# Kernel optimization log

Measured on AMD Instinct MI355X. Metric: run time of the kernel, lower is better.

The kernel has to match this reference:

```python
import jax, jax.numpy as jnp
import numpy as np

B, S, D_MODEL, N_HEADS, D_K, D_V = 32, 512, 256, 16, 16, 16


def setup_inputs() -> dict:
    key = jax.random.key(0)
    ks = jax.random.split(key, 9)
    def xavier(k, fan_in, fan_out):
        lim = np.sqrt(6.0 / (fan_in + fan_out)).astype(np.float32)
        return jax.random.uniform(k, (fan_out, fan_in), jnp.float32, -lim, lim)
    return {
        "Q": jax.random.normal(ks[0], (B, S, D_MODEL), jnp.float32),
        "K": jax.random.normal(ks[1], (B, S, D_MODEL), jnp.float32),
        "V": jax.random.normal(ks[2], (B, S, D_MODEL), jnp.float32),
        "mask": jnp.ones((B, S), jnp.float32),
        "W_Q": xavier(ks[3], D_MODEL, N_HEADS * D_K),
        "b_Q": jnp.zeros((N_HEADS * D_K,), jnp.float32),
        "W_K": xavier(ks[4], D_MODEL, N_HEADS * D_K),
        "b_K": jnp.zeros((N_HEADS * D_K,), jnp.float32),
        "W_V": xavier(ks[5], D_MODEL, N_HEADS * D_V),
        "b_V": jnp.zeros((N_HEADS * D_V,), jnp.float32),
    }


def reference(Q, K, V, mask, W_Q, b_Q, W_K, b_K, W_V, b_V):
    # Projections: torch Linear stores weight as (out, in) -> x @ W.T + b
    def proj(x, W, b, d):
        y = jnp.einsum('bsd,ed->bse', x, W) + b  # [B,S,H*d]
        return y.reshape(B, S, N_HEADS, d).transpose(0, 2, 1, 3)  # [B,H,S,d]
    q = proj(Q, W_Q, b_Q, D_K)
    k = proj(K, W_K, b_K, D_K)
    v = proj(V, W_V, b_V, D_V)
    # Unstabilized exp-score attention with multiplicative mask
    scores = jnp.exp(jnp.einsum('bhqd,bhkd->bhqk', q, k) / np.sqrt(D_K).astype(np.float32))
    scores = scores * mask[:, None, None, :]  # mask over key axis
    attn = scores / (jnp.sum(scores, axis=-1, keepdims=True) + 1e-8)
    ctx = jnp.einsum('bhqk,bhkd->bhqd', attn, v)  # [B,H,S,D_V]
    return ctx.transpose(0, 2, 1, 3).reshape(B, S, N_HEADS * D_V)
```

## Files before the change

kernel.cpp:

```cpp
#include <hip/hip_runtime.h>
#include <hip/hip_bf16.h>


#define PROJ_ELEMS (32 * 16 * 512 * 16)
#define LOG2E 1.44269504088896f

typedef _Float16 f16x4 __attribute__((ext_vector_type(4)));
typedef float    f32x4 __attribute__((ext_vector_type(4)));

static __device__ __forceinline__ f16x4 cvt4(float4 v) {
    f16x4 r;
    r[0] = (_Float16)v.x; r[1] = (_Float16)v.y;
    r[2] = (_Float16)v.z; r[3] = (_Float16)v.w;
    return r;
}

__global__ __launch_bounds__(256, 3) void proj_mfma(
    const float* __restrict__ Qx, const float* __restrict__ Kx, const float* __restrict__ Vx,
    const float* __restrict__ WQ, const float* __restrict__ bQ,
    const float* __restrict__ WK, const float* __restrict__ bK,
    const float* __restrict__ WV, const float* __restrict__ bV,
    _Float16* __restrict__ qh, _Float16* __restrict__ kh, _Float16* __restrict__ vth)
{
    const int proj = blockIdx.z;
    const float* __restrict__ X  = (proj == 0) ? Qx : (proj == 1) ? Kx : Vx;
    const float* __restrict__ W  = (proj == 0) ? WQ : (proj == 1) ? WK : WV;
    const float* __restrict__ bb = (proj == 0) ? bQ : (proj == 1) ? bK : bV;

    const int row0 = blockIdx.x * 64;
    const int t = threadIdx.x;
    const int w = t >> 6, l = t & 63;
    const int lm16 = l & 15, lg = l >> 4;

    __shared__ _Float16 xs[64][72];
    __shared__ _Float16 wsh[256][72];
    __shared__ float bl[256];

    bl[t] = bb[t];

    f32x4 acc[4][4];
#pragma unroll
    for (int mi = 0; mi < 4; mi++)
#pragma unroll
        for (int ni = 0; ni < 4; ni++) acc[mi][ni] = (f32x4){0.f, 0.f, 0.f, 0.f};

    for (int k0 = 0; k0 < 256; k0 += 64) {
        __syncthreads();
#pragma unroll
        for (int i = 0; i < 4; i++) {
            int f4 = t + i * 256;
            int r = f4 >> 4, kq = f4 & 15;
            float4 xv = *(const float4*)&X[(size_t)(row0 + r) * 256 + k0 + kq * 4];
            *(f16x4*)&xs[r][kq * 4] = cvt4(xv);
        }
#pragma unroll
        for (int i = 0; i < 16; i++) {
            int f4 = t + i * 256;
            int r = f4 >> 4, kq = f4 & 15;
            float4 wv = *(const float4*)&W[(size_t)r * 256 + k0 + kq * 4];
            *(f16x4*)&wsh[r][kq * 4] = cvt4(wv);
        }
        __syncthreads();

#pragma unroll
        for (int kq = 0; kq < 4; kq++) {
            f16x4 xf[4], wf[4];
#pragma unroll
            for (int mi = 0; mi < 4; mi++)
                xf[mi] = *(const f16x4*)&xs[mi * 16 + lm16][kq * 16 + lg * 4];
#pragma unroll
            for (int ni = 0; ni < 4; ni++)
                wf[ni] = *(const f16x4*)&wsh[w * 64 + ni * 16 + lm16][kq * 16 + lg * 4];

            if (proj < 2) {
#pragma unroll
                for (int mi = 0; mi < 4; mi++)
#pragma unroll
                    for (int ni = 0; ni < 4; ni++)
                        acc[mi][ni] = __builtin_amdgcn_mfma_f32_16x16x16f16(
                            wf[ni], xf[mi], acc[mi][ni], 0, 0, 0);
            } else {
#pragma unroll
                for (int mi = 0; mi < 4; mi++)
#pragma unroll
                    for (int ni = 0; ni < 4; ni++)
                        acc[mi][ni] = __builtin_amdgcn_mfma_f32_16x16x16f16(
                            xf[mi], wf[ni], acc[mi][ni], 0, 0, 0);
            }
        }
    }

    const int bq = row0 >> 9;
    const int sbase = row0 & 511;

    if (proj < 2) {
        const float scl = (proj == 0) ? 0.25f * LOG2E : 1.0f;
        _Float16* __restrict__ outp = (proj == 0) ? qh : kh;
#pragma unroll
        for (int mi = 0; mi < 4; mi++) {
            const int s = sbase + mi * 16 + lm16;
#pragma unroll
            for (int ni = 0; ni < 4; ni++) {
                const int col0 = w * 64 + ni * 16 + lg * 4;
                const int h = col0 >> 4, d0 = col0 & 15;
                _Float16 tmp[4];
#pragma unroll
                for (int r = 0; r < 4; r++)
                    tmp[r] = (_Float16)((acc[mi][ni][r] + bl[col0 + r]) * scl);
                *(f16x4*)&outp[(((size_t)bq * 16 + h) * 512 + s) * 16 + d0] =
                    *(const f16x4*)tmp;
            }
        }
    } else {
#pragma unroll
        for (int mi = 0; mi < 4; mi++) {
            const int s0 = sbase + mi * 16 + lg * 4;
#pragma unroll
            for (int ni = 0; ni < 4; ni++) {
                const int col = w * 64 + ni * 16 + lm16;
                const int h = col >> 4, d = col & 15;
                const float bc = bl[col];
                _Float16 tmp[4];
#pragma unroll
                for (int r = 0; r < 4; r++)
                    tmp[r] = (_Float16)(acc[mi][ni][r] + bc);
                *(f16x4*)&vth[(((size_t)bq * 16 + h) * 16 + d) * 512 + s0] =
                    *(const f16x4*)tmp;
            }
        }
    }
}

__global__ __launch_bounds__(256, 4) void attn_mfma(
    const _Float16* __restrict__ qh, const _Float16* __restrict__ kh,
    const _Float16* __restrict__ vth, const float* __restrict__ mask,
    float* __restrict__ out)
{
    const int blk  = blockIdx.x;
    const int bh   = blk >> 1;
    const int half = blk & 1;
    const int b = bh >> 4, h = bh & 15;

    __shared__ _Float16 ks[512 * 16];
    __shared__ _Float16 vt[16 * 528];
    __shared__ float    lm[512];
    __shared__ float    sums[256];

    const int t = threadIdx.x;
    const int w = t >> 6, l = t & 63;
    const int lm16 = l & 15, lg = l >> 4;

    {
        const float4* src = (const float4*)(kh + (size_t)bh * 8192);
        float4* dst = (float4*)ks;
#pragma unroll
        for (int i = 0; i < 4; i++) dst[t + i * 256] = src[t + i * 256];
    }
    {
        const _Float16* src = vth + (size_t)bh * 8192;
#pragma unroll
        for (int i = 0; i < 4; i++) {
            int f = t + i * 256;
            int d = f >> 6, c = f & 63;
            *(float4*)&vt[d * 528 + c * 8] = *(const float4*)&src[d * 512 + c * 8];
        }
    }
    {
#pragma unroll
        for (int i = 0; i < 2; i++) {
            int j = t + i * 256;
            lm[j] = __builtin_amdgcn_logf(mask[b * 512 + j]);
        }
    }

    f16x4 qf[4];
    {
        const _Float16* qb = qh + (size_t)bh * 8192;
#pragma unroll
        for (int mt = 0; mt < 4; mt++) {
            int m = half * 256 + w * 64 + mt * 16 + lm16;
            qf[mt] = *(const f16x4*)&qb[m * 16 + lg * 4];
        }
    }

    f32x4 acc[4];
    float rs[4];
#pragma unroll
    for (int mt = 0; mt < 4; mt++) {
        acc[mt] = (f32x4){0.f, 0.f, 0.f, 0.f};
        rs[mt] = 0.f;
    }

    __syncthreads();

    for (int jt = 0; jt < 32; jt++) {
        const int j0 = jt << 4;
        f16x4 ka = *(const f16x4*)&ks[(j0 + lm16) * 16 + lg * 4];
        f16x4 vb = *(const f16x4*)&vt[lm16 * 528 + j0 + lg * 4];
        f32x4 lmv = *(const f32x4*)&lm[j0 + lg * 4];
#pragma unroll
        for (int mt = 0; mt < 4; mt++) {
            f32x4 s4 = __builtin_amdgcn_mfma_f32_16x16x16f16(ka, qf[mt], lmv, 0, 0, 0);
            float e0 = __builtin_amdgcn_exp2f(s4[0]);
            float e1 = __builtin_amdgcn_exp2f(s4[1]);
            float e2 = __builtin_amdgcn_exp2f(s4[2]);
            float e3 = __builtin_amdgcn_exp2f(s4[3]);
            rs[mt] += (e0 + e1) + (e2 + e3);
            f16x4 pa;
            pa[0] = (_Float16)e0; pa[1] = (_Float16)e1;
            pa[2] = (_Float16)e2; pa[3] = (_Float16)e3;
            acc[mt] = __builtin_amdgcn_mfma_f32_16x16x16f16(pa, vb, acc[mt], 0, 0, 0);
        }
    }

#pragma unroll
    for (int mt = 0; mt < 4; mt++) {
        float r = rs[mt];
        r += __shfl_xor(r, 16);
        r += __shfl_xor(r, 32);
        if (l < 16) sums[w * 64 + mt * 16 + l] = r;
    }
    __syncthreads();

#pragma unroll
    for (int mt = 0; mt < 4; mt++) {
        f32x4 sv = *(const f32x4*)&sums[w * 64 + mt * 16 + lg * 4];
        int m = half * 256 + w * 64 + mt * 16 + lg * 4;
        float* o = out + ((size_t)(b * 512 + m) * 256) + h * 16 + lm16;
        o[0]   = acc[mt][0] / (sv[0] + 1e-8f);
        o[256] = acc[mt][1] / (sv[1] + 1e-8f);
        o[512] = acc[mt][2] / (sv[2] + 1e-8f);
        o[768] = acc[mt][3] / (sv[3] + 1e-8f);
    }
}

extern "C" void kernel_launch(void* const* d_in, const int* in_sizes, int n_in,
                              void* d_out, int out_size, void* d_ws, size_t ws_size,
                              hipStream_t stream) {
    const float* Q    = (const float*)d_in[0];
    const float* K    = (const float*)d_in[1];
    const float* V    = (const float*)d_in[2];
    const float* mask = (const float*)d_in[3];
    const float* W_Q  = (const float*)d_in[4];
    const float* b_Q  = (const float*)d_in[5];
    const float* W_K  = (const float*)d_in[6];
    const float* b_K  = (const float*)d_in[7];
    const float* W_V  = (const float*)d_in[8];
    const float* b_V  = (const float*)d_in[9];
    float* out = (float*)d_out;

    _Float16* qh  = (_Float16*)d_ws;
    _Float16* kh  = qh + PROJ_ELEMS;
    _Float16* vth = kh + PROJ_ELEMS;

    proj_mfma<<<dim3(256, 1, 3), 256, 0, stream>>>(
        Q, K, V, W_Q, b_Q, W_K, b_K, W_V, b_V, qh, kh, vth);

    attn_mfma<<<dim3(32 * 16 * 2), 256, 0, stream>>>(qh, kh, vth, mask, out);
}
```

Before: 182.5 us.

## Load projection operands directly from global memory into MFMA registers, dropping LDS staging

The projection GEMM no longer stages X and W tiles through shared memory with barriers. Each lane now loads its own MFMA fragments as float4 straight from global memory and converts them to fp16 in registers, and the bias is read from global in the epilogue. This removes the LDS write/read traffic and the __syncthreads calls. In exchange, each W element is loaded by every block with no sharing inside the block, the strided per-lane float4 loads coalesce less well, and register use grows (32 float4 per k-step), which is why launch bounds occupancy drops from 3 to 2.

Measured after the change: 180.6 us. About the same (-1.1%).

```diff
diff --git a/kernel.cpp b/kernel.cpp
--- a/kernel.cpp
+++ b/kernel.cpp
@@ -15,7 +15,7 @@
     return r;
 }
 
-__global__ __launch_bounds__(256, 3) void proj_mfma(
+__global__ __launch_bounds__(256, 2) void proj_mfma(
     const float* __restrict__ Qx, const float* __restrict__ Kx, const float* __restrict__ Vx,
     const float* __restrict__ WQ, const float* __restrict__ bQ,
     const float* __restrict__ WK, const float* __restrict__ bK,
@@ -32,11 +32,14 @@
     const int w = t >> 6, l = t & 63;
     const int lm16 = l & 15, lg = l >> 4;
 
-    __shared__ _Float16 xs[64][72];
-    __shared__ _Float16 wsh[256][72];
-    __shared__ float bl[256];
-
-    bl[t] = bb[t];
+    const float* xbase[4];
+    const float* wbase[4];
+#pragma unroll
+    for (int mi = 0; mi < 4; mi++)
+        xbase[mi] = X + (size_t)(row0 + mi * 16 + lm16) * 256 + lg * 4;
+#pragma unroll
+    for (int ni = 0; ni < 4; ni++)
+        wbase[ni] = W + (size_t)(w * 64 + ni * 16 + lm16) * 256 + lg * 4;
 
     f32x4 acc[4][4];
 #pragma unroll
@@ -44,33 +47,25 @@
 #pragma unroll
         for (int ni = 0; ni < 4; ni++) acc[mi][ni] = (f32x4){0.f, 0.f, 0.f, 0.f};
 
+#pragma unroll 1
     for (int k0 = 0; k0 < 256; k0 += 64) {
-        __syncthreads();
-#pragma unroll
-        for (int i = 0; i < 4; i++) {
-            int f4 = t + i * 256;
-            int r = f4 >> 4, kq = f4 & 15;
-            float4 xv = *(const float4*)&X[(size_t)(row0 + r) * 256 + k0 + kq * 4];
-            *(f16x4*)&xs[r][kq * 4] = cvt4(xv);
-        }
-#pragma unroll
-        for (int i = 0; i < 16; i++) {
-            int f4 = t + i * 256;
-            int r = f4 >> 4, kq = f4 & 15;
-            float4 wv = *(const float4*)&W[(size_t)r * 256 + k0 + kq * 4];
-            *(f16x4*)&wsh[r][kq * 4] = cvt4(wv);
-        }
-        __syncthreads();
-
+        float4 xr[4][4], wr[4][4];
+#pragma unroll
+        for (int kq = 0; kq < 4; kq++) {
+#pragma unroll
+            for (int mi = 0; mi < 4; mi++)
+                xr[kq][mi] = *(const float4*)(xbase[mi] + k0 + kq * 16);
+#pragma unroll
+            for (int ni = 0; ni < 4; ni++)
+                wr[kq][ni] = *(const float4*)(wbase[ni] + k0 + kq * 16);
+        }
 #pragma unroll
         for (int kq = 0; kq < 4; kq++) {
             f16x4 xf[4], wf[4];
 #pragma unroll
-            for (int mi = 0; mi < 4; mi++)
-                xf[mi] = *(const f16x4*)&xs[mi * 16 + lm16][kq * 16 + lg * 4];
-#pragma unroll
-            for (int ni = 0; ni < 4; ni++)
-                wf[ni] = *(const f16x4*)&wsh[w * 64 + ni * 16 + lm16][kq * 16 + lg * 4];
+            for (int mi = 0; mi < 4; mi++) xf[mi] = cvt4(xr[kq][mi]);
+#pragma unroll
+            for (int ni = 0; ni < 4; ni++) wf[ni] = cvt4(wr[kq][ni]);
 
             if (proj < 2) {
 #pragma unroll
@@ -103,10 +98,12 @@
             for (int ni = 0; ni < 4; ni++) {
                 const int col0 = w * 64 + ni * 16 + lg * 4;
                 const int h = col0 >> 4, d0 = col0 & 15;
+                const float4 bv = *(const float4*)&bb[col0];
                 _Float16 tmp[4];
-#pragma unroll
-                for (int r = 0; r < 4; r++)
-                    tmp[r] = (_Float16)((acc[mi][ni][r] + bl[col0 + r]) * scl);
+                tmp[0] = (_Float16)((acc[mi][ni][0] + bv.x) * scl);
+                tmp[1] = (_Float16)((acc[mi][ni][1] + bv.y) * scl);
+                tmp[2] = (_Float16)((acc[mi][ni][2] + bv.z) * scl);
+                tmp[3] = (_Float16)((acc[mi][ni][3] + bv.w) * scl);
                 *(f16x4*)&outp[(((size_t)bq * 16 + h) * 512 + s) * 16 + d0] =
                     *(const f16x4*)tmp;
             }
@@ -119,7 +116,7 @@
             for (int ni = 0; ni < 4; ni++) {
                 const int col = w * 64 + ni * 16 + lm16;
                 const int h = col >> 4, d = col & 15;
-                const float bc = bl[col];
+                const float bc = bb[col];
                 _Float16 tmp[4];
 #pragma unroll
                 for (int r = 0; r < 4; r++)
```
